# Optimization experiments

Measured on AMD Instinct MI355X. Metric: run time of the kernel, lower is better.

The kernel has to match this reference:

```python
import jax, jax.numpy as jnp
import numpy as np

B, S, D, H, E, FF = 8, 512, 768, 12, 8, 3072
HD = D // H

def layernorm(x, g, b, eps=1e-5):
    mu = jnp.mean(x, axis=-1, keepdims=True)
    var = jnp.mean((x - mu) ** 2, axis=-1, keepdims=True)
    return (x - mu) * jax.lax.rsqrt(var + eps) * g + b

def setup_inputs() -> dict:
    key = jax.random.key(0)
    ks = jax.random.split(key, 16)
    sd = lambda n: 1.0 / np.sqrt(n)
    return {
        "x": jax.random.normal(ks[0], (B, S, D), jnp.float32),
        "indexes_list": jax.random.randint(ks[1], (1,), 0, E),
        "ln1_g": jnp.ones((D,), jnp.float32),
        "ln1_b": jnp.zeros((D,), jnp.float32),
        "qkv_w": jax.random.normal(ks[2], (D, 3 * D), jnp.float32) * sd(D),
        "proj_w": jax.random.normal(ks[3], (D, D), jnp.float32) * sd(D),
        "proj_b": jnp.zeros((D,), jnp.float32),
        "ln2_g": jnp.ones((D,), jnp.float32),
        "ln2_b": jnp.zeros((D,), jnp.float32),
        "switch_w": jax.random.normal(ks[4], (D, E), jnp.float32) * sd(D),
        "switch_b": jnp.zeros((E,), jnp.float32),
        "w1": jax.random.normal(ks[5], (E, D, FF), jnp.float32) * sd(D),
        "b1": jnp.zeros((E, FF), jnp.float32),
        "w2": jax.random.normal(ks[6], (E, FF, D), jnp.float32) * sd(FF),
        "b2": jnp.zeros((E, D), jnp.float32),
    }

def reference(x, indexes_list, ln1_g, ln1_b, qkv_w, proj_w, proj_b,
              ln2_g, ln2_b, switch_w, switch_b, w1, b1, w2, b2):
    # --- attention sublayer ---
    h = layernorm(x, ln1_g, ln1_b)
    qkv = (h @ qkv_w).reshape(B, S, 3, H, HD).transpose(2, 0, 3, 1, 4)  # [3,B,H,S,hd]
    q, k, v = qkv[0], qkv[1], qkv[2]
    scale = HD ** -0.5
    attn = jax.nn.softmax(jnp.einsum('bhqd,bhkd->bhqk', q, k) * scale, axis=-1)
    o = jnp.einsum('bhqk,bhkd->bhqd', attn, v).transpose(0, 2, 1, 3).reshape(B, S, D)
    x = x + o @ proj_w + proj_b
    # --- switch MoE sublayer (routes arg ignored, as in original) ---
    h = layernorm(x, ln2_g, ln2_b).reshape(B * S, D)  # [T,D]
    logits = h @ switch_w + switch_b
    routes = jnp.argmax(jax.nn.softmax(logits, axis=-1), axis=-1)  # [T]
    # dense per-expert compute, then select by route (same math as gather/scatter)
    y = jax.nn.gelu(jnp.einsum('td,edf->etf', h, w1) + b1[:, None, :], approximate=False)
    y = jax.nn.gelu(jnp.einsum('etf,efd->etd', y, w2) + b2[:, None, :], approximate=False)
    moe_out = y[routes, jnp.arange(B * S)]  # [T,D]
    return x + moe_out.reshape(B, S, D)
```

## Files before the change

### kernel.cpp

```cpp
#include <hip/hip_runtime.h>
#include <math.h>

#define T_TOK   4096
#define D_MODEL 768
#define H_HEADS 12
#define HDIM    64
#define S_SEQ   512
#define B_BATCH 8
#define E_EXP   8
#define FF_DIM  3072
#define MAX_TILES 40
#define MPAD_MAX  (MAX_TILES * 128)

typedef __attribute__((ext_vector_type(8))) short short8;
typedef __attribute__((ext_vector_type(4))) float floatx4;

__device__ __forceinline__ float gelu_exact(float x) {
    return 0.5f * x * (1.0f + erff(x * 0.7071067811865476f));
}

__device__ __forceinline__ unsigned short f2bf(float f) {
    unsigned int u = __float_as_uint(f);
    u += 0x7fffu + ((u >> 16) & 1u);
    return (unsigned short)(u >> 16);
}
__device__ __forceinline__ float bf2f(unsigned short h) {
    return __uint_as_float(((unsigned int)h) << 16);
}
__device__ __forceinline__ void split_bf(float v, unsigned short& hi, unsigned short& lo) {
    hi = f2bf(v);
    lo = f2bf(v - bf2f(hi));
}

__device__ __forceinline__ void gload16(const void* g, void* l) {
    __builtin_amdgcn_global_load_lds(
        (const __attribute__((address_space(1))) unsigned int*)g,
        (__attribute__((address_space(3))) unsigned int*)l, 16, 0, 0);
}
__device__ __forceinline__ int swz3(int r) { return (r ^ (r >> 2)) & 3; }

__global__ void __launch_bounds__(256) ln_f32(const float* __restrict__ x,
                                              const float* __restrict__ g,
                                              const float* __restrict__ b,
                                              float* __restrict__ out) {
    int row = blockIdx.x;
    const float* xr = x + (size_t)row * D_MODEL;
    int tid = threadIdx.x;
    float v0 = xr[tid], v1 = xr[tid + 256], v2 = xr[tid + 512];
    float s = v0 + v1 + v2;
    float q = v0 * v0 + v1 * v1 + v2 * v2;
    for (int off = 32; off; off >>= 1) {
        s += __shfl_down(s, off);
        q += __shfl_down(q, off);
    }
    __shared__ float rs[4], rq[4], stats[2];
    int wid = tid >> 6, lane = tid & 63;
    if (lane == 0) { rs[wid] = s; rq[wid] = q; }
    __syncthreads();
    if (tid == 0) {
        float ts = rs[0] + rs[1] + rs[2] + rs[3];
        float tq = rq[0] + rq[1] + rq[2] + rq[3];
        float mu = ts * (1.0f / 768.0f);
        float var = tq * (1.0f / 768.0f) - mu * mu;
        stats[0] = mu; stats[1] = rsqrtf(var + 1e-5f);
    }
    __syncthreads();
    float mu = stats[0], rstd = stats[1];
    float* orow = out + (size_t)row * D_MODEL;
    orow[tid]       = (v0 - mu) * rstd * g[tid]       + b[tid];
    orow[tid + 256] = (v1 - mu) * rstd * g[tid + 256] + b[tid + 256];
    orow[tid + 512] = (v2 - mu) * rstd * g[tid + 512] + b[tid + 512];
}

__global__ void __launch_bounds__(256) ln_split(const float* __restrict__ x,
                                                const float* __restrict__ g,
                                                const float* __restrict__ b,
                                                unsigned short* __restrict__ ohi,
                                                unsigned short* __restrict__ olo) {
    int row = blockIdx.x;
    const float* xr = x + (size_t)row * D_MODEL;
    int tid = threadIdx.x;
    float v0 = xr[tid], v1 = xr[tid + 256], v2 = xr[tid + 512];
    float s = v0 + v1 + v2;
    float q = v0 * v0 + v1 * v1 + v2 * v2;
    for (int off = 32; off; off >>= 1) {
        s += __shfl_down(s, off);
        q += __shfl_down(q, off);
    }
    __shared__ float rs[4], rq[4], stats[2];
    int wid = tid >> 6, lane = tid & 63;
    if (lane == 0) { rs[wid] = s; rq[wid] = q; }
    __syncthreads();
    if (tid == 0) {
        float ts = rs[0] + rs[1] + rs[2] + rs[3];
        float tq = rq[0] + rq[1] + rq[2] + rq[3];
        float mu = ts * (1.0f / 768.0f);
        float var = tq * (1.0f / 768.0f) - mu * mu;
        stats[0] = mu; stats[1] = rsqrtf(var + 1e-5f);
    }
    __syncthreads();
    float mu = stats[0], rstd = stats[1];
    unsigned short* hr = ohi + (size_t)row * D_MODEL;
    unsigned short* lr = olo + (size_t)row * D_MODEL;
    float r0 = (v0 - mu) * rstd * g[tid]       + b[tid];
    float r1 = (v1 - mu) * rstd * g[tid + 256] + b[tid + 256];
    float r2 = (v2 - mu) * rstd * g[tid + 512] + b[tid + 512];
    unsigned short hi, lo;
    split_bf(r0, hi, lo); hr[tid] = hi;       lr[tid] = lo;
    split_bf(r1, hi, lo); hr[tid + 256] = hi; lr[tid + 256] = lo;
    split_bf(r2, hi, lo); hr[tid + 512] = hi; lr[tid + 512] = lo;
}

__global__ void __launch_bounds__(256) transpose_bf16(const float* __restrict__ in,
                                                      unsigned short* __restrict__ out,
                                                      int R, int C) {
    __shared__ float t[32][33];
    const float* inb = in + (size_t)blockIdx.z * R * C;
    unsigned short* outb = out + (size_t)blockIdx.z * R * C;
    int c0 = blockIdx.x * 32, r0 = blockIdx.y * 32;
    int tx = threadIdx.x & 31, ty = threadIdx.x >> 5;
#pragma unroll
    for (int rr = 0; rr < 32; rr += 8)
        t[ty + rr][tx] = inb[(size_t)(r0 + ty + rr) * C + c0 + tx];
    __syncthreads();
#pragma unroll
    for (int rr = 0; rr < 32; rr += 8)
        outb[(size_t)(c0 + ty + rr) * R + r0 + tx] = f2bf(t[tx][ty + rr]);
}

__global__ void __launch_bounds__(256) transpose_split(const float* __restrict__ in,
                                                       unsigned short* __restrict__ out_hi,
                                                       unsigned short* __restrict__ out_lo,
                                                       int R, int C) {
    __shared__ float t[32][33];
    int c0 = blockIdx.x * 32, r0 = blockIdx.y * 32;
    int tx = threadIdx.x & 31, ty = threadIdx.x >> 5;
#pragma unroll
    for (int rr = 0; rr < 32; rr += 8)
        t[ty + rr][tx] = in[(size_t)(r0 + ty + rr) * C + c0 + tx];
    __syncthreads();
#pragma unroll
    for (int rr = 0; rr < 32; rr += 8) {
        float v = t[tx][ty + rr];
        unsigned short hi, lo;
        split_bf(v, hi, lo);
        size_t idx = (size_t)(c0 + ty + rr) * R + r0 + tx;
        out_hi[idx] = hi;
        out_lo[idx] = lo;
    }
}

__global__ void __launch_bounds__(256) attn_mfma(const float* __restrict__ qkv,
                                                 unsigned short* __restrict__ ohi,
                                                 unsigned short* __restrict__ olo) {
    __shared__ __align__(16) short Kh[64][72], Kl[64][72];
    __shared__ __align__(16) short Vh[64][72], Vl[64][72];

    int qt = blockIdx.x, hh = blockIdx.y, bb = blockIdx.z;
    int tid = threadIdx.x;
    int lane = tid & 63, wv = tid >> 6;
    int lm = lane & 15, q8 = (lane >> 4) * 8, q4 = (lane >> 4) * 4;
    const size_t rstride = 3 * D_MODEL;
    const float* base = qkv + (size_t)bb * S_SEQ * rstride + hh * HDIM;

    short8 qh[2], ql[2];
    {
        const float* qrow = base + (size_t)(qt * 64 + 16 * wv + lm) * rstride;
#pragma unroll
        for (int ks = 0; ks < 2; ks++) {
            float4 v0 = *(const float4*)(qrow + ks * 32 + q8);
            float4 v1 = *(const float4*)(qrow + ks * 32 + q8 + 4);
            unsigned short h_, l_;
            short8 sh, sl;
            split_bf(v0.x * 0.125f, h_, l_); sh[0] = (short)h_; sl[0] = (short)l_;
            split_bf(v0.y * 0.125f, h_, l_); sh[1] = (short)h_; sl[1] = (short)l_;
            split_bf(v0.z * 0.125f, h_, l_); sh[2] = (short)h_; sl[2] = (short)l_;
            split_bf(v0.w * 0.125f, h_, l_); sh[3] = (short)h_; sl[3] = (short)l_;
            split_bf(v1.x * 0.125f, h_, l_); sh[4] = (short)h_; sl[4] = (short)l_;
            split_bf(v1.y * 0.125f, h_, l_); sh[5] = (short)h_; sl[5] = (short)l_;
            split_bf(v1.z * 0.125f, h_, l_); sh[6] = (short)h_; sl[6] = (short)l_;
            split_bf(v1.w * 0.125f, h_, l_); sh[7] = (short)h_; sl[7] = (short)l_;
            qh[ks] = sh; ql[ks] = sl;
        }
    }

    float m_run[4], l_run[4];
    floatx4 o_acc[4];
#pragma unroll
    for (int i = 0; i < 4; i++) {
        m_run[i] = -1e30f; l_run[i] = 0.f;
        o_acc[i] = (floatx4){0.f, 0.f, 0.f, 0.f};
    }

    int sr = tid >> 2;
    int sc0 = (tid & 3) * 16;

    for (int kt = 0; kt < 8; kt++) {
        __syncthreads();
        {
            const float* krow = base + (size_t)(kt * 64 + sr) * rstride + D_MODEL;
            const float* vrow = krow + D_MODEL;
#pragma unroll
            for (int c = 0; c < 16; c += 4) {
                float4 kv = *(const float4*)(krow + sc0 + c);
                ushort4 h4, l4; unsigned short h_, l_;
                split_bf(kv.x, h_, l_); h4.x = h_; l4.x = l_;
                split_bf(kv.y, h_, l_); h4.y = h_; l4.y = l_;
                split_bf(kv.z, h_, l_); h4.z = h_; l4.z = l_;
                split_bf(kv.w, h_, l_); h4.w = h_; l4.w = l_;
                *(ushort4*)&Kh[sr][sc0 + c] = h4;
                *(ushort4*)&Kl[sr][sc0 + c] = l4;
                float4 vv = *(const float4*)(vrow + sc0 + c);
                split_bf(vv.x, h_, l_); Vh[sc0 + c + 0][sr] = (short)h_; Vl[sc0 + c + 0][sr] = (short)l_;
                split_bf(vv.y, h_, l_); Vh[sc0 + c + 1][sr] = (short)h_; Vl[sc0 + c + 1][sr] = (short)l_;
                split_bf(vv.z, h_, l_); Vh[sc0 + c + 2][sr] = (short)h_; Vl[sc0 + c + 2][sr] = (short)l_;
                split_bf(vv.w, h_, l_); Vh[sc0 + c + 3][sr] = (short)h_; Vl[sc0 + c + 3][sr] = (short)l_;
            }
        }
        __syncthreads();

        floatx4 s_acc[4];
#pragma unroll
        for (int nt = 0; nt < 4; nt++) s_acc[nt] = (floatx4){0.f, 0.f, 0.f, 0.f};
#pragma unroll
        for (int ks = 0; ks < 2; ks++) {
#pragma unroll
            for (int nt = 0; nt < 4; nt++) {
                short8 bh = *(const short8*)&Kh[nt * 16 + lm][ks * 32 + q8];
                short8 bl = *(const short8*)&Kl[nt * 16 + lm][ks * 32 + q8];
                s_acc[nt] = __builtin_amdgcn_mfma_f32_16x16x32_bf16(qh[ks], bh, s_acc[nt], 0, 0, 0);
                s_acc[nt] = __builtin_amdgcn_mfma_f32_16x16x32_bf16(qh[ks], bl, s_acc[nt], 0, 0, 0);
                s_acc[nt] = __builtin_amdgcn_mfma_f32_16x16x32_bf16(ql[ks], bh, s_acc[nt], 0, 0, 0);
            }
        }

        float alpha_r[4];
#pragma unroll
        for (int reg = 0; reg < 4; reg++) {
            float tm = fmaxf(fmaxf(s_acc[0][reg], s_acc[1][reg]),
                             fmaxf(s_acc[2][reg], s_acc[3][reg]));
            tm = fmaxf(tm, __shfl_xor(tm, 1));
            tm = fmaxf(tm, __shfl_xor(tm, 2));
            tm = fmaxf(tm, __shfl_xor(tm, 4));
            tm = fmaxf(tm, __shfl_xor(tm, 8));
            float mn = fmaxf(m_run[reg], tm);
            alpha_r[reg] = __expf(m_run[reg] - mn);
            m_run[reg] = mn;
            float ts = 0.f;
#pragma unroll
            for (int nt = 0; nt < 4; nt++) {
                float pv = __expf(s_acc[nt][reg] - mn);
                s_acc[nt][reg] = pv;
                ts += pv;
            }
            ts += __shfl_xor(ts, 1);
            ts += __shfl_xor(ts, 2);
            ts += __shfl_xor(ts, 4);
            ts += __shfl_xor(ts, 8);
            l_run[reg] = l_run[reg] * alpha_r[reg] + ts;
        }

        __syncthreads();

#pragma unroll
        for (int nt = 0; nt < 4; nt++)
#pragma unroll
            for (int reg = 0; reg < 4; reg++) {
                unsigned short h_, l_;
                split_bf(s_acc[nt][reg], h_, l_);
                Kh[16 * wv + q4 + reg][nt * 16 + lm] = (short)h_;
                Kl[16 * wv + q4 + reg][nt * 16 + lm] = (short)l_;
            }
#pragma unroll
        for (int nt = 0; nt < 4; nt++)
#pragma unroll
            for (int reg = 0; reg < 4; reg++) o_acc[nt][reg] *= alpha_r[reg];

        __syncthreads();

#pragma unroll
        for (int ks = 0; ks < 2; ks++) {
            short8 ph = *(const short8*)&Kh[16 * wv + lm][ks * 32 + q8];
            short8 pl = *(const short8*)&Kl[16 * wv + lm][ks * 32 + q8];
#pragma unroll
            for (int nt = 0; nt < 4; nt++) {
                short8 vh = *(const short8*)&Vh[nt * 16 + lm][ks * 32 + q8];
                short8 vl = *(const short8*)&Vl[nt * 16 + lm][ks * 32 + q8];
                o_acc[nt] = __builtin_amdgcn_mfma_f32_16x16x32_bf16(ph, vh, o_acc[nt], 0, 0, 0);
                o_acc[nt] = __builtin_amdgcn_mfma_f32_16x16x32_bf16(ph, vl, o_acc[nt], 0, 0, 0);
                o_acc[nt] = __builtin_amdgcn_mfma_f32_16x16x32_bf16(pl, vh, o_acc[nt], 0, 0, 0);
            }
        }
    }

    size_t ob = (size_t)(bb * S_SEQ + qt * 64) * D_MODEL + hh * HDIM;
#pragma unroll
    for (int reg = 0; reg < 4; reg++) {
        float inv = 1.0f / l_run[reg];
#pragma unroll
        for (int nt = 0; nt < 4; nt++) {
            unsigned short h_, l_;
            split_bf(o_acc[nt][reg] * inv, h_, l_);
            size_t idx = ob + (size_t)(16 * wv + q4 + reg) * D_MODEL + nt * 16 + lm;
            ohi[idx] = h_;
            olo[idx] = l_;
        }
    }
}

__global__ void __launch_bounds__(64) router_kernel(const float* __restrict__ h2,
                                                    const float* __restrict__ sw,
                                                    const float* __restrict__ sb,
                                                    int* __restrict__ routes,
                                                    int* __restrict__ counts) {
    int t = blockIdx.x;
    int lane = threadIdx.x;
    const float* hr = h2 + (size_t)t * D_MODEL;
    float acc[8] = {};
    for (int d = lane; d < D_MODEL; d += 64) {
        float hv = hr[d];
        const float* wr = sw + (size_t)d * 8;
#pragma unroll
        for (int e = 0; e < 8; e++) acc[e] += hv * wr[e];
    }
#pragma unroll
    for (int e = 0; e < 8; e++)
        for (int off = 32; off; off >>= 1) acc[e] += __shfl_down(acc[e], off);
    if (lane == 0) {
        int best = 0;
        float bv = acc[0] + sb[0];
#pragma unroll
        for (int e = 1; e < 8; e++) {
            float v = acc[e] + sb[e];
            if (v > bv) { bv = v; best = e; }
        }
        routes[t] = best;
        atomicAdd(&counts[best], 1);
    }
}

__global__ void __launch_bounds__(256) init_kernel(int* counts, int* cursor, int* perm) {
    int idx = blockIdx.x * 256 + threadIdx.x;
    if (idx < MPAD_MAX) perm[idx] = -1;
    if (idx < 8) { counts[idx] = 0; cursor[idx] = 0; }
}

__global__ void moe_plan(const int* __restrict__ counts, int* pad_base,
                         int* tile_e, int* tile_row0, int* ntiles) {
    if (threadIdx.x == 0 && blockIdx.x == 0) {
        int base = 0, nt = 0;
        for (int e = 0; e < E_EXP; e++) {
            pad_base[e] = base;
            int c = counts[e];
            int nte = (c + 127) >> 7;
            for (int j = 0; j < nte; j++) {
                tile_e[nt] = e;
                tile_row0[nt] = base + j * 128;
                nt++;
            }
            base += nte * 128;
        }
        ntiles[0] = nt;
    }
}

__global__ void __launch_bounds__(256) scatter_kernel(const int* __restrict__ routes,
                                                      const int* __restrict__ pad_base,
                                                      int* __restrict__ cursor,
                                                      int* __restrict__ perm) {
    int t = blockIdx.x * 256 + threadIdx.x;
    if (t < T_TOK) {
        int e = routes[t];
        int pos = atomicAdd(&cursor[e], 1);
        perm[pad_base[e] + pos] = t;
    }
}

__global__ void __launch_bounds__(256) gather_bf16(const float* __restrict__ h2,
                                                   const int* __restrict__ perm,
                                                   unsigned short* __restrict__ Ag) {
    int g = blockIdx.x;
    int row = perm[g];
    unsigned short* dst = Ag + (size_t)g * D_MODEL;
    if (row >= 0) {
        const float* src = h2 + (size_t)row * D_MODEL;
        for (int d = threadIdx.x; d < D_MODEL; d += 256) dst[d] = f2bf(src[d]);
    } else {
        for (int d = threadIdx.x; d < D_MODEL; d += 256) dst[d] = 0;
    }
}

template <int MODE>
__global__ void __launch_bounds__(256) sgemm(const unsigned short* __restrict__ Ah_,
                                             const unsigned short* __restrict__ Al_,
                                             const unsigned short* __restrict__ Bh_,
                                             const unsigned short* __restrict__ Bl_,
                                             const float* __restrict__ bias,
                                             const float* __restrict__ resid,
                                             float* __restrict__ Cf,
                                             int N, int K) {
    __shared__ __align__(16) short Ah[128][32];
    __shared__ __align__(16) short Al[128][32];
    __shared__ __align__(16) short Bh[128][32];
    __shared__ __align__(16) short Bl[128][32];

    int row0 = blockIdx.y * 128, n0 = blockIdx.x * 128;
    int tid = threadIdx.x;
    int lane = tid & 63, wid = tid >> 6;
    int wr0 = (wid >> 1) * 64, wc0 = (wid & 1) * 64;
    int lm = lane & 15, q8 = (lane >> 4) * 8;

    int rch = lane >> 2, sl = lane & 3;
    int rst = wid * 32 + rch;
    int gsb = (sl ^ swz3(rst)) << 4;
    short* lA0 = &Ah[wid * 32][0];
    short* lA1 = &Ah[wid * 32 + 16][0];
    short* lL0 = &Al[wid * 32][0];
    short* lL1 = &Al[wid * 32 + 16][0];
    short* lB0 = &Bh[wid * 32][0];
    short* lB1 = &Bh[wid * 32 + 16][0];
    short* lM0 = &Bl[wid * 32][0];
    short* lM1 = &Bl[wid * 32 + 16][0];

    floatx4 acc[4][4];
#pragma unroll
    for (int i = 0; i < 4; i++)
#pragma unroll
        for (int j = 0; j < 4; j++) acc[i][j] = (floatx4){0.f, 0.f, 0.f, 0.f};

    const unsigned short* Ahb = Ah_ + (size_t)row0 * K;
    const unsigned short* Alb = Al_ + (size_t)row0 * K;
    const unsigned short* Bhb = Bh_ + (size_t)n0 * K;
    const unsigned short* Blb = Bl_ + (size_t)n0 * K;

    size_t ro0 = (size_t)rst * K;
    size_t ro1 = ro0 + (size_t)16 * K;

    for (int k0 = 0; k0 < K; k0 += 32) {
        gload16((const char*)(Ahb + ro0 + k0) + gsb, lA0);
        gload16((const char*)(Ahb + ro1 + k0) + gsb, lA1);
        gload16((const char*)(Alb + ro0 + k0) + gsb, lL0);
        gload16((const char*)(Alb + ro1 + k0) + gsb, lL1);
        gload16((const char*)(Bhb + ro0 + k0) + gsb, lB0);
        gload16((const char*)(Bhb + ro1 + k0) + gsb, lB1);
        gload16((const char*)(Blb + ro0 + k0) + gsb, lM0);
        gload16((const char*)(Blb + ro1 + k0) + gsb, lM1);
        __syncthreads();

        short8 ah[4], al[4], bh[4], bl[4];
#pragma unroll
        for (int i = 0; i < 4; i++) {
            int r = wr0 + i * 16 + lm;
            int bo = (q8 * 2) ^ (swz3(r) << 4);
            ah[i] = *(const short8*)((const char*)&Ah[r][0] + bo);
            al[i] = *(const short8*)((const char*)&Al[r][0] + bo);
        }
#pragma unroll
        for (int j = 0; j < 4; j++) {
            int r = wc0 + j * 16 + lm;
            int bo = (q8 * 2) ^ (swz3(r) << 4);
            bh[j] = *(const short8*)((const char*)&Bh[r][0] + bo);
            bl[j] = *(const short8*)((const char*)&Bl[r][0] + bo);
        }
#pragma unroll
        for (int i = 0; i < 4; i++)
#pragma unroll
            for (int j = 0; j < 4; j++) {
                acc[i][j] = __builtin_amdgcn_mfma_f32_16x16x32_bf16(ah[i], bh[j], acc[i][j], 0, 0, 0);
                acc[i][j] = __builtin_amdgcn_mfma_f32_16x16x32_bf16(ah[i], bl[j], acc[i][j], 0, 0, 0);
                acc[i][j] = __builtin_amdgcn_mfma_f32_16x16x32_bf16(al[i], bh[j], acc[i][j], 0, 0, 0);
            }
        __syncthreads();
    }

    int q4 = (lane >> 4) * 4;
#pragma unroll
    for (int i = 0; i < 4; i++) {
#pragma unroll
        for (int j = 0; j < 4; j++) {
            int c = n0 + wc0 + j * 16 + lm;
#pragma unroll
            for (int reg = 0; reg < 4; reg++) {
                int rloc = wr0 + i * 16 + q4 + reg;
                size_t idx = (size_t)(row0 + rloc) * N + c;
                float v = acc[i][j][reg];
                if constexpr (MODE == 0) Cf[idx] = v;
                else                     Cf[idx] = resid[idx] + v + bias[c];
            }
        }
    }
}

template <int MODE>
__global__ void __launch_bounds__(256) mgemm(const unsigned short* __restrict__ A,
                                             const unsigned short* __restrict__ Bt,
                                             const float* __restrict__ bias,
                                             const float* __restrict__ resid,
                                             float* __restrict__ Cf,
                                             unsigned short* __restrict__ Cb,
                                             int N, int K,
                                             const int* __restrict__ perm,
                                             const int* __restrict__ tile_e,
                                             const int* __restrict__ tile_row0,
                                             const int* __restrict__ ntiles) {
    __shared__ __align__(16) short As[128][32];
    __shared__ __align__(16) short Bs[128][32];

    if ((int)blockIdx.y >= ntiles[0]) return;
    int e = tile_e[blockIdx.y];
    int row0 = tile_row0[blockIdx.y];
    Bt += (size_t)e * N * K;
    bias += (size_t)e * N;
    int n0 = blockIdx.x * 128;

    int tid = threadIdx.x;
    int lane = tid & 63, wid = tid >> 6;
    int wr0 = (wid >> 1) * 64, wc0 = (wid & 1) * 64;
    int lm = lane & 15, q8 = (lane >> 4) * 8;

    int rch = lane >> 2, sl = lane & 3;
    int rst = wid * 32 + rch;
    int gsb = (sl ^ swz3(rst)) << 4;
    short* lA0 = &As[wid * 32][0];
    short* lA1 = &As[wid * 32 + 16][0];
    short* lB0 = &Bs[wid * 32][0];
    short* lB1 = &Bs[wid * 32 + 16][0];

    floatx4 acc[4][4];
#pragma unroll
    for (int i = 0; i < 4; i++)
#pragma unroll
        for (int j = 0; j < 4; j++) acc[i][j] = (floatx4){0.f, 0.f, 0.f, 0.f};

    const unsigned short* Abase = A + (size_t)row0 * K;
    const unsigned short* Bbase = Bt + (size_t)n0 * K;

    size_t ro0 = (size_t)rst * K;
    size_t ro1 = ro0 + (size_t)16 * K;

    for (int k0 = 0; k0 < K; k0 += 32) {
        gload16((const char*)(Abase + ro0 + k0) + gsb, lA0);
        gload16((const char*)(Abase + ro1 + k0) + gsb, lA1);
        gload16((const char*)(Bbase + ro0 + k0) + gsb, lB0);
        gload16((const char*)(Bbase + ro1 + k0) + gsb, lB1);
        __syncthreads();

        short8 af[4], bfr[4];
#pragma unroll
        for (int i = 0; i < 4; i++) {
            int r = wr0 + i * 16 + lm;
            int bo = (q8 * 2) ^ (swz3(r) << 4);
            af[i] = *(const short8*)((const char*)&As[r][0] + bo);
        }
#pragma unroll
        for (int j = 0; j < 4; j++) {
            int r = wc0 + j * 16 + lm;
            int bo = (q8 * 2) ^ (swz3(r) << 4);
            bfr[j] = *(const short8*)((const char*)&Bs[r][0] + bo);
        }
#pragma unroll
        for (int i = 0; i < 4; i++)
#pragma unroll
            for (int j = 0; j < 4; j++)
                acc[i][j] = __builtin_amdgcn_mfma_f32_16x16x32_bf16(af[i], bfr[j], acc[i][j], 0, 0, 0);
        __syncthreads();
    }

    int q4 = (lane >> 4) * 4;
#pragma unroll
    for (int i = 0; i < 4; i++) {
#pragma unroll
        for (int j = 0; j < 4; j++) {
            int c = n0 + wc0 + j * 16 + lm;
#pragma unroll
            for (int reg = 0; reg < 4; reg++) {
                int rloc = wr0 + i * 16 + q4 + reg;
                float v = acc[i][j][reg];
                if constexpr (MODE == 2) {
                    Cb[(size_t)(row0 + rloc) * N + c] = f2bf(gelu_exact(v + bias[c]));
                } else {
                    int t = perm[row0 + rloc];
                    if (t >= 0) {
                        size_t idx = (size_t)t * N + c;
                        Cf[idx] = resid[idx] + gelu_exact(v + bias[c]);
                    }
                }
            }
        }
    }
}

extern "C" void kernel_launch(void* const* d_in, const int* in_sizes, int n_in,
                              void* d_out, int out_size, void* d_ws, size_t ws_size,
                              hipStream_t stream) {
    const float* x      = (const float*)d_in[0];
    const float* ln1_g  = (const float*)d_in[2];
    const float* ln1_b  = (const float*)d_in[3];
    const float* qkv_w  = (const float*)d_in[4];
    const float* proj_w = (const float*)d_in[5];
    const float* proj_b = (const float*)d_in[6];
    const float* ln2_g  = (const float*)d_in[7];
    const float* ln2_b  = (const float*)d_in[8];
    const float* sw     = (const float*)d_in[9];
    const float* sb     = (const float*)d_in[10];
    const float* w1     = (const float*)d_in[11];
    const float* b1     = (const float*)d_in[12];
    const float* w2     = (const float*)d_in[13];
    const float* b2     = (const float*)d_in[14];
    float* out = (float*)d_out;

    char* p = (char*)d_ws;
    float*          qkv = (float*)p;
    float*          h   = (float*)p;
    unsigned short* y1  = (unsigned short*)p;
    p += (size_t)T_TOK * 2304 * 4;
    unsigned short* h_hi = (unsigned short*)p; p += (size_t)T_TOK * D_MODEL * 2;
    unsigned short* h_lo = (unsigned short*)p; p += (size_t)T_TOK * D_MODEL * 2;
    unsigned short* o_hi = h_hi;
    unsigned short* o_lo = h_lo;
    float* x1 = (float*)p; p += (size_t)T_TOK * D_MODEL * 4;
    unsigned short* Ag     = (unsigned short*)p;
    unsigned short* qwt_hi = (unsigned short*)p;
    unsigned short* qwt_lo = qwt_hi + (size_t)2304 * 768;
    p += (size_t)MPAD_MAX * D_MODEL * 2;
    unsigned short* pwt_hi = (unsigned short*)p; p += (size_t)768 * 768 * 2;
    unsigned short* pwt_lo = (unsigned short*)p; p += (size_t)768 * 768 * 2;
    unsigned short* w1t = (unsigned short*)p; p += (size_t)E_EXP * 3072 * 768 * 2;
    unsigned short* w2t = (unsigned short*)p; p += (size_t)E_EXP * 768 * 3072 * 2;
    int* routes    = (int*)p;
    int* perm      = routes + T_TOK;
    int* counts    = perm + MPAD_MAX;
    int* cursor    = counts + 8;
    int* pad_base  = cursor + 8;
    int* tile_e    = pad_base + 8;
    int* tile_row0 = tile_e + MAX_TILES;
    int* ntiles    = tile_row0 + MAX_TILES;

    transpose_split<<<dim3(2304 / 32, 768 / 32), 256, 0, stream>>>(qkv_w, qwt_hi, qwt_lo, 768, 2304);
    transpose_split<<<dim3(768 / 32, 768 / 32), 256, 0, stream>>>(proj_w, pwt_hi, pwt_lo, 768, 768);
    transpose_bf16<<<dim3(3072 / 32, 768 / 32, 8), 256, 0, stream>>>(w1, w1t, 768, 3072);
    transpose_bf16<<<dim3(768 / 32, 3072 / 32, 8), 256, 0, stream>>>(w2, w2t, 3072, 768);

    ln_split<<<T_TOK, 256, 0, stream>>>(x, ln1_g, ln1_b, h_hi, h_lo);
    sgemm<0><<<dim3(2304 / 128, T_TOK / 128), 256, 0, stream>>>(
        h_hi, h_lo, qwt_hi, qwt_lo, nullptr, nullptr, qkv, 2304, 768);
    attn_mfma<<<dim3(S_SEQ / 64, H_HEADS, B_BATCH), 256, 0, stream>>>(qkv, o_hi, o_lo);
    sgemm<1><<<dim3(768 / 128, T_TOK / 128), 256, 0, stream>>>(
        o_hi, o_lo, pwt_hi, pwt_lo, proj_b, x, x1, 768, 768);
    ln_f32<<<T_TOK, 256, 0, stream>>>(x1, ln2_g, ln2_b, h);
    init_kernel<<<(MPAD_MAX + 255) / 256, 256, 0, stream>>>(counts, cursor, perm);
    router_kernel<<<T_TOK, 64, 0, stream>>>(h, sw, sb, routes, counts);
    moe_plan<<<1, 1, 0, stream>>>(counts, pad_base, tile_e, tile_row0, ntiles);
    scatter_kernel<<<T_TOK / 256, 256, 0, stream>>>(routes, pad_base, cursor, perm);
    gather_bf16<<<MPAD_MAX, 256, 0, stream>>>(h, perm, Ag);
    mgemm<2><<<dim3(FF_DIM / 128, MAX_TILES), 256, 0, stream>>>(
        Ag, w1t, b1, nullptr, nullptr, y1, FF_DIM, 768,
        perm, tile_e, tile_row0, ntiles);
    mgemm<3><<<dim3(D_MODEL / 128, MAX_TILES), 256, 0, stream>>>(
        y1, w2t, b2, x1, out, nullptr, D_MODEL, 3072,
        perm, tile_e, tile_row0, ntiles);
}
```

Baseline: 636.4 us.

## Double-buffer LDS tiles in sgemm and mgemm, widen mgemm K-step to 64

```diff
diff --git a/kernel.cpp b/kernel.cpp
--- a/kernel.cpp
+++ b/kernel.cpp
@@ -399,10 +399,10 @@
                                              const float* __restrict__ resid,
                                              float* __restrict__ Cf,
                                              int N, int K) {
-    __shared__ __align__(16) short Ah[128][32];
-    __shared__ __align__(16) short Al[128][32];
-    __shared__ __align__(16) short Bh[128][32];
-    __shared__ __align__(16) short Bl[128][32];
+    __shared__ __align__(16) short Ah[2][128][32];
+    __shared__ __align__(16) short Al[2][128][32];
+    __shared__ __align__(16) short Bh[2][128][32];
+    __shared__ __align__(16) short Bl[2][128][32];
 
     int row0 = blockIdx.y * 128, n0 = blockIdx.x * 128;
     int tid = threadIdx.x;
@@ -413,54 +413,58 @@
     int rch = lane >> 2, sl = lane & 3;
     int rst = wid * 32 + rch;
     int gsb = (sl ^ swz3(rst)) << 4;
-    short* lA0 = &Ah[wid * 32][0];
-    short* lA1 = &Ah[wid * 32 + 16][0];
-    short* lL0 = &Al[wid * 32][0];
-    short* lL1 = &Al[wid * 32 + 16][0];
-    short* lB0 = &Bh[wid * 32][0];
-    short* lB1 = &Bh[wid * 32 + 16][0];
-    short* lM0 = &Bl[wid * 32][0];
-    short* lM1 = &Bl[wid * 32 + 16][0];
-
-    floatx4 acc[4][4];
-#pragma unroll
-    for (int i = 0; i < 4; i++)
-#pragma unroll
-        for (int j = 0; j < 4; j++) acc[i][j] = (floatx4){0.f, 0.f, 0.f, 0.f};
 
     const unsigned short* Ahb = Ah_ + (size_t)row0 * K;
     const unsigned short* Alb = Al_ + (size_t)row0 * K;
     const unsigned short* Bhb = Bh_ + (size_t)n0 * K;
     const unsigned short* Blb = Bl_ + (size_t)n0 * K;
 
-    size_t ro0 = (size_t)rst * K;
-    size_t ro1 = ro0 + (size_t)16 * K;
-
-    for (int k0 = 0; k0 < K; k0 += 32) {
-        gload16((const char*)(Ahb + ro0 + k0) + gsb, lA0);
-        gload16((const char*)(Ahb + ro1 + k0) + gsb, lA1);
-        gload16((const char*)(Alb + ro0 + k0) + gsb, lL0);
-        gload16((const char*)(Alb + ro1 + k0) + gsb, lL1);
-        gload16((const char*)(Bhb + ro0 + k0) + gsb, lB0);
-        gload16((const char*)(Bhb + ro1 + k0) + gsb, lB1);
-        gload16((const char*)(Blb + ro0 + k0) + gsb, lM0);
-        gload16((const char*)(Blb + ro1 + k0) + gsb, lM1);
-        __syncthreads();
+    const char* gAh = (const char*)(Ahb + (size_t)rst * K) + gsb;
+    const char* gAl = (const char*)(Alb + (size_t)rst * K) + gsb;
+    const char* gBh = (const char*)(Bhb + (size_t)rst * K) + gsb;
+    const char* gBl = (const char*)(Blb + (size_t)rst * K) + gsb;
+    size_t r16 = (size_t)16 * K * 2;
+
+    auto stage = [&](int b, int t) {
+        size_t kb = (size_t)t * 64;
+        gload16(gAh + kb,       &Ah[b][wid * 32][0]);
+        gload16(gAh + r16 + kb, &Ah[b][wid * 32 + 16][0]);
+        gload16(gAl + kb,       &Al[b][wid * 32][0]);
+        gload16(gAl + r16 + kb, &Al[b][wid * 32 + 16][0]);
+        gload16(gBh + kb,       &Bh[b][wid * 32][0]);
+        gload16(gBh + r16 + kb, &Bh[b][wid * 32 + 16][0]);
+        gload16(gBl + kb,       &Bl[b][wid * 32][0]);
+        gload16(gBl + r16 + kb, &Bl[b][wid * 32 + 16][0]);
+    };
+
+    floatx4 acc[4][4];
+#pragma unroll
+    for (int i = 0; i < 4; i++)
+#pragma unroll
+        for (int j = 0; j < 4; j++) acc[i][j] = (floatx4){0.f, 0.f, 0.f, 0.f};
+
+    const int NSTEP = K >> 5;
+    stage(0, 0);
+    __syncthreads();
+
+    int cur = 0;
+    for (int t = 0; t < NSTEP; t++) {
+        if (t + 1 < NSTEP) stage(cur ^ 1, t + 1);
 
         short8 ah[4], al[4], bh[4], bl[4];
 #pragma unroll
         for (int i = 0; i < 4; i++) {
             int r = wr0 + i * 16 + lm;
             int bo = (q8 * 2) ^ (swz3(r) << 4);
-            ah[i] = *(const short8*)((const char*)&Ah[r][0] + bo);
-            al[i] = *(const short8*)((const char*)&Al[r][0] + bo);
+            ah[i] = *(const short8*)((const char*)&Ah[cur][r][0] + bo);
+            al[i] = *(const short8*)((const char*)&Al[cur][r][0] + bo);
         }
 #pragma unroll
         for (int j = 0; j < 4; j++) {
             int r = wc0 + j * 16 + lm;
             int bo = (q8 * 2) ^ (swz3(r) << 4);
-            bh[j] = *(const short8*)((const char*)&Bh[r][0] + bo);
-            bl[j] = *(const short8*)((const char*)&Bl[r][0] + bo);
+            bh[j] = *(const short8*)((const char*)&Bh[cur][r][0] + bo);
+            bl[j] = *(const short8*)((const char*)&Bl[cur][r][0] + bo);
         }
 #pragma unroll
         for (int i = 0; i < 4; i++)
@@ -471,6 +475,7 @@
                 acc[i][j] = __builtin_amdgcn_mfma_f32_16x16x32_bf16(al[i], bh[j], acc[i][j], 0, 0, 0);
             }
         __syncthreads();
+        cur ^= 1;
     }
 
     int q4 = (lane >> 4) * 4;
@@ -503,8 +508,8 @@
                                              const int* __restrict__ tile_e,
                                              const int* __restrict__ tile_row0,
                                              const int* __restrict__ ntiles) {
-    __shared__ __align__(16) short As[128][32];
-    __shared__ __align__(16) short Bs[128][32];
+    __shared__ __align__(16) short As[2][128][64];
+    __shared__ __align__(16) short Bs[2][128][64];
 
     if ((int)blockIdx.y >= ntiles[0]) return;
     int e = tile_e[blockIdx.y];
@@ -518,52 +523,60 @@
     int wr0 = (wid >> 1) * 64, wc0 = (wid & 1) * 64;
     int lm = lane & 15, q8 = (lane >> 4) * 8;
 
-    int rch = lane >> 2, sl = lane & 3;
-    int rst = wid * 32 + rch;
-    int gsb = (sl ^ swz3(rst)) << 4;
-    short* lA0 = &As[wid * 32][0];
-    short* lA1 = &As[wid * 32 + 16][0];
-    short* lB0 = &Bs[wid * 32][0];
-    short* lB1 = &Bs[wid * 32 + 16][0];
-
-    floatx4 acc[4][4];
-#pragma unroll
-    for (int i = 0; i < 4; i++)
-#pragma unroll
-        for (int j = 0; j < 4; j++) acc[i][j] = (floatx4){0.f, 0.f, 0.f, 0.f};
+    int rl = lane >> 3, sl = lane & 7;
+    int gsb = (sl ^ rl) << 4;
 
     const unsigned short* Abase = A + (size_t)row0 * K;
     const unsigned short* Bbase = Bt + (size_t)n0 * K;
-
-    size_t ro0 = (size_t)rst * K;
-    size_t ro1 = ro0 + (size_t)16 * K;
-
-    for (int k0 = 0; k0 < K; k0 += 32) {
-        gload16((const char*)(Abase + ro0 + k0) + gsb, lA0);
-        gload16((const char*)(Abase + ro1 + k0) + gsb, lA1);
-        gload16((const char*)(Bbase + ro0 + k0) + gsb, lB0);
-        gload16((const char*)(Bbase + ro1 + k0) + gsb, lB1);
+    const char* gA = (const char*)(Abase + (size_t)(wid * 32 + rl) * K) + gsb;
+    const char* gB = (const char*)(Bbase + (size_t)(wid * 32 + rl) * K) + gsb;
+
+    auto stage = [&](int b, int t) {
+        size_t kb = (size_t)t * 128;
+#pragma unroll
+        for (int c = 0; c < 4; c++) {
+            gload16(gA + (size_t)c * 16 * K + kb, &As[b][wid * 32 + c * 8][0]);
+            gload16(gB + (size_t)c * 16 * K + kb, &Bs[b][wid * 32 + c * 8][0]);
+        }
+    };
+
+    floatx4 acc[4][4];
+#pragma unroll
+    for (int i = 0; i < 4; i++)
+#pragma unroll
+        for (int j = 0; j < 4; j++) acc[i][j] = (floatx4){0.f, 0.f, 0.f, 0.f};
+
+    const int NSTEP = K >> 6;
+    stage(0, 0);
+    __syncthreads();
+
+    int cur = 0;
+    for (int t = 0; t < NSTEP; t++) {
+        if (t + 1 < NSTEP) stage(cur ^ 1, t + 1);
+
+#pragma unroll
+        for (int ks = 0; ks < 2; ks++) {
+            short8 af[4], bfr[4];
+#pragma unroll
+            for (int i = 0; i < 4; i++) {
+                int r = wr0 + i * 16 + lm;
+                int bo = (ks * 64 + q8 * 2) ^ ((r & 7) << 4);
+                af[i] = *(const short8*)((const char*)&As[cur][r][0] + bo);
+            }
+#pragma unroll
+            for (int j = 0; j < 4; j++) {
+                int r = wc0 + j * 16 + lm;
+                int bo = (ks * 64 + q8 * 2) ^ ((r & 7) << 4);
+                bfr[j] = *(const short8*)((const char*)&Bs[cur][r][0] + bo);
+            }
+#pragma unroll
+            for (int i = 0; i < 4; i++)
+#pragma unroll
+                for (int j = 0; j < 4; j++)
+                    acc[i][j] = __builtin_amdgcn_mfma_f32_16x16x32_bf16(af[i], bfr[j], acc[i][j], 0, 0, 0);
+        }
         __syncthreads();
-
-        short8 af[4], bfr[4];
-#pragma unroll
-        for (int i = 0; i < 4; i++) {
-            int r = wr0 + i * 16 + lm;
-            int bo = (q8 * 2) ^ (swz3(r) << 4);
-            af[i] = *(const short8*)((const char*)&As[r][0] + bo);
-        }
-#pragma unroll
-        for (int j = 0; j < 4; j++) {
-            int r = wc0 + j * 16 + lm;
-            int bo = (q8 * 2) ^ (swz3(r) << 4);
-            bfr[j] = *(const short8*)((const char*)&Bs[r][0] + bo);
-        }
-#pragma unroll
-        for (int i = 0; i < 4; i++)
-#pragma unroll
-            for (int j = 0; j < 4; j++)
-                acc[i][j] = __builtin_amdgcn_mfma_f32_16x16x32_bf16(af[i], bfr[j], acc[i][j], 0, 0, 0);
-        __syncthreads();
+        cur ^= 1;
     }
 
     int q4 = (lane >> 4) * 4;
```

New measurement: 617.0 us. 1.03x faster.
